# Performance work log

Measured on AMD Instinct MI355X. Metric: run time of the kernel, lower is better.

## Reference

```python
import jax, jax.numpy as jnp
import numpy as np

B, T, D = 4, 1024, 1024
H, DH = 16, 64
SCALE = 1.0 / (DH ** 0.5)


def skew(QE):
    # QE: [B, H, T, 2T-1] -> relative-position skew (Music Transformer)
    b, h, t, _ = QE.shape
    QE = jnp.pad(QE, ((0, 0), (0, 0), (0, 0), (0, 1))).reshape(b, h, 2 * t * t)
    QE = jnp.pad(QE, ((0, 0), (0, 0), (0, t - 1))).reshape(b, h, t + 1, 2 * t - 1)
    return QE[:, :, :t, -t:]


def setup_inputs() -> dict:
    key = jax.random.key(0)
    ks = jax.random.split(key, 11)
    s = 0.02
    return {
        "x": jax.random.normal(ks[0], (B, T, D), jnp.float32),
        "context": jax.random.normal(ks[1], (B, T, D), jnp.float32),
        "mask": jax.random.randint(ks[2], (B, 1, T, T), 0, 2).astype(jnp.bool_),
        "lookup_table": jax.random.normal(ks[3], (2 * T - 1, DH), jnp.float32) * s,
        "Wq": jax.random.normal(ks[4], (D, H * DH), jnp.float32) * s,
        "Wk": jax.random.normal(ks[5], (D, H * DH), jnp.float32) * s,
        "Wv": jax.random.normal(ks[6], (D, H * DH), jnp.float32) * s,
        "Wo": jax.random.normal(ks[7], (H * DH, D), jnp.float32) * s,
        "bo": jnp.zeros((D,), jnp.float32),
        "gamma": jnp.ones((D,), jnp.float32),
        "beta": jnp.zeros((D,), jnp.float32),
    }


def reference(x, context, mask, lookup_table, Wq, Wk, Wv, Wo, bo, gamma, beta):
    b, t, d = x.shape
    # projections -> [B, H, T, DH]
    q = (x @ Wq).reshape(b, t, H, DH).transpose(0, 2, 1, 3)
    k = (context @ Wk).reshape(b, t, H, DH).transpose(0, 2, 1, 3)
    v = (context @ Wv).reshape(b, t, H, DH).transpose(0, 2, 1, 3)

    score = jnp.einsum("bhqd,bhkd->bhqk", q, k)
    score = score + skew(jnp.einsum("bhqd,rd->bhqr", q, lookup_table))
    score = score * SCALE
    score = jnp.where(mask, jnp.float32(-1e9), score)
    attn = jax.nn.softmax(score, axis=-1)

    out = jnp.einsum("bhqk,bhkd->bhqd", attn, v)
    out = out.transpose(0, 2, 1, 3).reshape(b, t, H * DH)
    out = out @ Wo + bo  # dropout is identity at inference (p effectively 0)

    y = x + out
    mu = jnp.mean(y, axis=-1, keepdims=True)
    var = jnp.var(y, axis=-1, keepdims=True)
    return (y - mu) / jnp.sqrt(var + 1e-5) * gamma + beta
```

## Files before the change

kernel.cpp:

```cpp
#include <hip/hip_runtime.h>

#define Tn 1024
#define Hn 16
#define Dn 1024
#define DHn 64
#define QSCALE 0.18033688011112042f

typedef unsigned short u16;
typedef unsigned long long ull;
typedef __bf16 bf16x8 __attribute__((ext_vector_type(8)));
typedef float f32x4 __attribute__((ext_vector_type(4)));

__device__ __forceinline__ u16 f2bf(float f) {
  union { float f; unsigned u; } v; v.f = f;
  return (u16)((v.u + 0x7FFFu + ((v.u >> 16) & 1u)) >> 16);
}
__device__ __forceinline__ float bf2f(u16 s) {
  union { unsigned u; float f; } v; v.u = ((unsigned)s) << 16;
  return v.f;
}
__device__ __forceinline__ f32x4 mfma16(bf16x8 a, bf16x8 b, f32x4 c) {
  return __builtin_amdgcn_mfma_f32_16x16x32_bf16(a, b, c, 0, 0, 0);
}

__global__ void k_convert(const float* __restrict__ src, u16* __restrict__ dst, int n) {
  int i = (blockIdx.x * blockDim.x + threadIdx.x) * 4;
  if (i >= n) return;
  float4 v = *(const float4*)(src + i);
  union { u16 s[4]; uint2 u; } o;
  o.s[0] = f2bf(v.x); o.s[1] = f2bf(v.y); o.s[2] = f2bf(v.z); o.s[3] = f2bf(v.w);
  *(uint2*)(dst + i) = o.u;
}

__global__ __launch_bounds__(256) void k_maskpack(const unsigned char* __restrict__ m,
                                                  unsigned long long* __restrict__ mb) {
  int wi = blockIdx.x * 4 + (threadIdx.x >> 6);
  int lane = threadIdx.x & 63;
  unsigned char v = m[((size_t)wi << 6) + lane];
  unsigned long long bal = __ballot(v != 0);
  if (lane == 0) mb[wi] = bal;
}

__global__ void k_transpose_convert(const float* __restrict__ W, u16* __restrict__ Wt) {
  __shared__ float tile[32][33];
  int n0 = blockIdx.x * 32, k0 = blockIdx.y * 32;
  int tx = threadIdx.x, ty = threadIdx.y;
  #pragma unroll
  for (int i = 0; i < 4; i++)
    tile[ty + 8*i][tx] = W[(size_t)(k0 + ty + 8*i) * Dn + n0 + tx];
  __syncthreads();
  #pragma unroll
  for (int i = 0; i < 4; i++)
    Wt[(size_t)(n0 + ty + 8*i) * Dn + k0 + tx] = f2bf(tile[tx][ty + 8*i]);
}

__global__ __launch_bounds__(256) void k_proj(const float* __restrict__ x, const float* __restrict__ ctxI,
                                              const u16* __restrict__ WqT, const u16* __restrict__ WkvT,
                                              u16* __restrict__ Qb, u16* __restrict__ Kb, u16* __restrict__ Vb) {
  __shared__ __align__(16) u16 Al[128][40];
  __shared__ __align__(16) u16 Bl[128][40];
  int bx = blockIdx.x;
  bool isQ = bx < 256;
  int idx = isQ ? bx : bx - 256;
  int m0 = (idx & 31) * 128;
  int n0 = (idx >> 5) * 128;
  const float* A = isQ ? x : ctxI;
  const u16* Bt = isQ ? WqT : WkvT;
  u16* dst0 = isQ ? Qb : Kb;
  float scale = isQ ? QSCALE : 1.0f;
  int tid = threadIdx.x;
  int w = tid >> 6, lane = tid & 63, g = lane >> 4, lr = lane & 15;
  int wr = w >> 1, wc = w & 1;
  f32x4 acc[4][4] = {};
  int sr = tid >> 2, sc = tid & 3;
  const float* Ap0 = &A[(size_t)(m0 + sr) * Dn + sc * 8];
  const float* Ap1 = Ap0 + (size_t)64 * Dn;
  const u16* Bp0 = &Bt[(size_t)(n0 + sr) * Dn + sc * 8];
  const u16* Bp1 = Bp0 + (size_t)64 * Dn;
  float4 ra0a = *(const float4*)Ap0, ra0b = *(const float4*)(Ap0 + 4);
  float4 ra1a = *(const float4*)Ap1, ra1b = *(const float4*)(Ap1 + 4);
  int4 rb0 = *(const int4*)Bp0;
  int4 rb1 = *(const int4*)Bp1;
  for (int k0 = 0; k0 < Dn; k0 += 32) {
    __syncthreads();
    {
      union { u16 s[8]; int4 v; } c0, c1;
      c0.s[0]=f2bf(ra0a.x); c0.s[1]=f2bf(ra0a.y); c0.s[2]=f2bf(ra0a.z); c0.s[3]=f2bf(ra0a.w);
      c0.s[4]=f2bf(ra0b.x); c0.s[5]=f2bf(ra0b.y); c0.s[6]=f2bf(ra0b.z); c0.s[7]=f2bf(ra0b.w);
      c1.s[0]=f2bf(ra1a.x); c1.s[1]=f2bf(ra1a.y); c1.s[2]=f2bf(ra1a.z); c1.s[3]=f2bf(ra1a.w);
      c1.s[4]=f2bf(ra1b.x); c1.s[5]=f2bf(ra1b.y); c1.s[6]=f2bf(ra1b.z); c1.s[7]=f2bf(ra1b.w);
      *(int4*)&Al[sr][sc*8]      = c0.v;
      *(int4*)&Al[sr + 64][sc*8] = c1.v;
    }
    *(int4*)&Bl[sr][sc*8]      = rb0;
    *(int4*)&Bl[sr + 64][sc*8] = rb1;
    __syncthreads();
    if (k0 + 32 < Dn) {
      ra0a = *(const float4*)(Ap0 + k0 + 32); ra0b = *(const float4*)(Ap0 + k0 + 36);
      ra1a = *(const float4*)(Ap1 + k0 + 32); ra1b = *(const float4*)(Ap1 + k0 + 36);
      rb0 = *(const int4*)(Bp0 + k0 + 32);
      rb1 = *(const int4*)(Bp1 + k0 + 32);
    }
    bf16x8 a[4], b[4];
    #pragma unroll
    for (int mi = 0; mi < 4; mi++) a[mi] = *(const bf16x8*)&Al[wr*64 + mi*16 + lr][g*8];
    #pragma unroll
    for (int ni = 0; ni < 4; ni++) b[ni] = *(const bf16x8*)&Bl[wc*64 + ni*16 + lr][g*8];
    #pragma unroll
    for (int mi = 0; mi < 4; mi++)
      #pragma unroll
      for (int ni = 0; ni < 4; ni++)
        acc[mi][ni] = mfma16(a[mi], b[ni], acc[mi][ni]);
  }
  #pragma unroll
  for (int mi = 0; mi < 4; mi++)
    #pragma unroll
    for (int ni = 0; ni < 4; ni++) {
      int row0 = m0 + wr*64 + mi*16 + g*4;
      int col = n0 + wc*64 + ni*16 + lr;
      int bb = row0 >> 10, tt0 = row0 & 1023;
      int hh = col >> 6, dd = col & 63;
      if (hh < 16) {
        u16* p = dst0 + (((size_t)(bb*16 + hh) << 10) + (size_t)tt0) * 64 + dd;
        #pragma unroll
        for (int r = 0; r < 4; r++) p[(size_t)r * 64] = f2bf(acc[mi][ni][r] * scale);
      } else {
        union { u16 s[4]; uint2 u; } o;
        #pragma unroll
        for (int r = 0; r < 4; r++) o.s[r] = f2bf(acc[mi][ni][r]);
        *(uint2*)(Vb + (((size_t)((bb*16 + (hh - 16)) * 64 + dd)) << 10) + tt0) = o.u;
      }
    }
}

__global__ __launch_bounds__(256) void k_gemm_bt(const u16* __restrict__ A, const u16* __restrict__ Bt,
                                                 u16* __restrict__ dst0, const float* __restrict__ bias) {
  __shared__ __align__(16) u16 Al[128][40];
  __shared__ __align__(16) u16 Bl[128][40];
  int m0 = blockIdx.y * 128, n0 = blockIdx.x * 128;
  int tid = threadIdx.x;
  int w = tid >> 6, lane = tid & 63, g = lane >> 4, lr = lane & 15;
  int wr = w >> 1, wc = w & 1;
  f32x4 acc[4][4] = {};
  int sr = tid >> 2, sc = tid & 3;
  const u16* Ap0 = &A[(size_t)(m0 + sr) * Dn + sc * 8];
  const u16* Ap1 = &A[(size_t)(m0 + sr + 64) * Dn + sc * 8];
  const u16* Bp0 = &Bt[(size_t)(n0 + sr) * Dn + sc * 8];
  const u16* Bp1 = &Bt[(size_t)(n0 + sr + 64) * Dn + sc * 8];
  int4 ra0 = *(const int4*)Ap0;
  int4 ra1 = *(const int4*)Ap1;
  int4 rb0 = *(const int4*)Bp0;
  int4 rb1 = *(const int4*)Bp1;
  for (int k0 = 0; k0 < Dn; k0 += 32) {
    __syncthreads();
    *(int4*)&Al[sr][sc*8]      = ra0;
    *(int4*)&Al[sr + 64][sc*8] = ra1;
    *(int4*)&Bl[sr][sc*8]      = rb0;
    *(int4*)&Bl[sr + 64][sc*8] = rb1;
    __syncthreads();
    if (k0 + 32 < Dn) {
      ra0 = *(const int4*)(Ap0 + k0 + 32);
      ra1 = *(const int4*)(Ap1 + k0 + 32);
      rb0 = *(const int4*)(Bp0 + k0 + 32);
      rb1 = *(const int4*)(Bp1 + k0 + 32);
    }
    bf16x8 a[4], b[4];
    #pragma unroll
    for (int mi = 0; mi < 4; mi++) a[mi] = *(const bf16x8*)&Al[wr*64 + mi*16 + lr][g*8];
    #pragma unroll
    for (int ni = 0; ni < 4; ni++) b[ni] = *(const bf16x8*)&Bl[wc*64 + ni*16 + lr][g*8];
    #pragma unroll
    for (int mi = 0; mi < 4; mi++)
      #pragma unroll
      for (int ni = 0; ni < 4; ni++)
        acc[mi][ni] = mfma16(a[mi], b[ni], acc[mi][ni]);
  }
  #pragma unroll
  for (int mi = 0; mi < 4; mi++)
    #pragma unroll
    for (int ni = 0; ni < 4; ni++) {
      int row0 = m0 + wr*64 + mi*16 + g*4;
      int col = n0 + wc*64 + ni*16 + lr;
      #pragma unroll
      for (int r = 0; r < 4; r++)
        dst0[(size_t)(row0 + r) * Dn + col] = f2bf(acc[mi][ni][r] + bias[col]);
    }
}

__global__ __launch_bounds__(512, 2) void k_attn(const u16* __restrict__ Qb, const u16* __restrict__ Kb,
                                              const u16* __restrict__ VT, const u16* __restrict__ Eb,
                                              const unsigned long long* __restrict__ mbits,
                                              u16* __restrict__ ctx) {
  __shared__ __align__(16) u16 KlF[128 * 64];
  __shared__ __align__(16) u16 Vt[64][136];
  __shared__ __align__(16) u16 RP[8][16][72];
  int h = blockIdx.y;
  int b = blockIdx.x;
  int q0 = blockIdx.z * 256;
  int tid = threadIdx.x;
  int w = tid >> 6, lane = tid & 63, g = lane >> 4, lr = lane & 15;
  int qw0 = q0 + w * 32;
  size_t headoff = (size_t)(b * Hn + h) * Tn * DHn;
  bf16x8 qf0 = *(const bf16x8*)&Qb[headoff + (size_t)(qw0 + lr)*64 + g*8];
  bf16x8 qf1 = *(const bf16x8*)&Qb[headoff + (size_t)(qw0 + lr)*64 + 32 + g*8];
  bf16x8 qf2 = *(const bf16x8*)&Qb[headoff + (size_t)(qw0 + 16 + lr)*64 + g*8];
  bf16x8 qf3 = *(const bf16x8*)&Qb[headoff + (size_t)(qw0 + 16 + lr)*64 + 32 + g*8];
  f32x4 O[8] = {};
  f32x4 Os0 = {0.f, 0.f, 0.f, 0.f}, Os1 = {0.f, 0.f, 0.f, 0.f};
  union { u16 s[8]; bf16x8 v; } one8;
  #pragma unroll
  for (int j = 0; j < 8; j++) one8.s[j] = 0x3F80u;

  int srcl[4]; bool psel[4];
  #pragma unroll
  for (int r = 0; r < 4; r++) {
    int rowq = g*4 + r;
    srcl[r] = (lane & 48) + ((lr - rowq + 15) & 15);
    psel[r] = (lr <= rowq);
  }
  const unsigned long long* mrow = mbits + ((size_t)(b * Tn + qw0 + g*4) << 4);

  f32x4 carry0 = {0.f, 0.f, 0.f, 0.f}, carry1 = {0.f, 0.f, 0.f, 0.f};
  {
    int rm = 1008 - qw0;
    const u16* ep = &Eb[(size_t)(rm + lr) * 64 + g*8];
    carry0 = mfma16(qf0, *(const bf16x8*)ep, carry0);
    carry0 = mfma16(qf1, *(const bf16x8*)(ep + 32), carry0);
    const u16* ep1 = &Eb[(size_t)(rm - 16 + lr) * 64 + g*8];
    carry1 = mfma16(qf2, *(const bf16x8*)ep1, carry1);
    carry1 = mfma16(qf3, *(const bf16x8*)(ep1 + 32), carry1);
  }

  int sKr = tid >> 3, sKc = (tid & 7) * 8;
  int kswz = sKc ^ ((sKr & 7) << 3);
  int sVr = tid >> 4, sVc = (tid & 15) * 8;
  const u16* Kgs = Kb + headoff + (size_t)sKr * 64 + sKc;
  const u16* Vgs = VT + headoff + (size_t)sVr * 1024 + sVc;
  int4 kA = *(const int4*)Kgs;
  int4 kB = *(const int4*)(Kgs + (size_t)64 * 64);
  int4 vA = *(const int4*)Vgs;
  int4 vB = *(const int4*)(Vgs + 32 * 1024);

  int kread = (g * 8) ^ ((lr & 7) << 3);
  int kread2 = (32 + g * 8) ^ ((lr & 7) << 3);

  for (int k0 = 0; k0 < Tn; k0 += 128) {
    __syncthreads();
    *(int4*)&KlF[sKr * 64 + kswz]        = kA;
    *(int4*)&KlF[(sKr + 64) * 64 + kswz] = kB;
    *(int4*)&Vt[sVr][sVc]                = vA;
    *(int4*)&Vt[sVr + 32][sVc]           = vB;
    __syncthreads();

    uint2 mw0[2][4], mw1[2][4];
    #pragma unroll
    for (int t = 0; t < 2; t++)
      #pragma unroll
      for (int r = 0; r < 4; r++) {
        mw0[t][r] = *(const uint2*)(mrow + (size_t)r * 16 + (k0 >> 6) + t);
        mw1[t][r] = *(const uint2*)(mrow + 256 + (size_t)r * 16 + (k0 >> 6) + t);
      }

    int rmin0 = k0 - qw0 + 1008;
    bf16x8 pa000, pa001, pa010, pa011;
    bf16x8 pa100, pa101, pa110, pa111;

    bf16x8 e0[5][2];
    #pragma unroll
    for (int j = 0; j < 5; j++) {
      const u16* ep = &Eb[(size_t)(rmin0 + j*16 + lr) * 64 + g*8];
      e0[j][0] = *(const bf16x8*)ep;
      e0[j][1] = *(const bf16x8*)(ep + 32);
    }
    f32x4 Rm0[5], Rn0[5];
    Rm0[0] = carry0;
    Rn0[0] = carry1;
    __builtin_amdgcn_s_setprio(1);
    #pragma unroll
    for (int j = 1; j < 5; j++) {
      f32x4 R = {0.f, 0.f, 0.f, 0.f};
      R = mfma16(qf0, e0[j][0], R);
      R = mfma16(qf1, e0[j][1], R);
      Rm0[j] = R;
      f32x4 R2 = {0.f, 0.f, 0.f, 0.f};
      R2 = mfma16(qf2, e0[j-1][0], R2);
      R2 = mfma16(qf3, e0[j-1][1], R2);
      Rn0[j] = R2;
    }
    f32x4 S0[4], T0[4];
    #pragma unroll
    for (int c = 0; c < 4; c++) {
      int krow = c*16 + lr;
      bf16x8 kf0 = *(const bf16x8*)&KlF[krow*64 + kread];
      bf16x8 kf1 = *(const bf16x8*)&KlF[krow*64 + kread2];
      f32x4 z = {0.f, 0.f, 0.f, 0.f};
      z = mfma16(qf0, kf0, z); z = mfma16(qf1, kf1, z);
      S0[c] = z;
      f32x4 z2 = {0.f, 0.f, 0.f, 0.f};
      z2 = mfma16(qf2, kf0, z2); z2 = mfma16(qf3, kf1, z2);
      T0[c] = z2;
    }
    __builtin_amdgcn_s_setprio(0);
    {
      float sh[5][4], si[5][4];
      #pragma unroll
      for (int s5 = 0; s5 < 5; s5++)
        #pragma unroll
        for (int r = 0; r < 4; r++) {
          sh[s5][r] = __shfl(Rm0[s5][r], srcl[r], 64);
          si[s5][r] = __shfl(Rn0[s5][r], srcl[r], 64);
        }
      #pragma unroll
      for (int c = 0; c < 4; c++)
        #pragma unroll
        for (int r = 0; r < 4; r++) {
          float s = S0[c][r] + (psel[r] ? sh[c][r] : sh[c+1][r]);
          unsigned bit;
          if (c == 0)      bit = (mw0[0][r].x >> lr) & 1u;
          else if (c == 1) bit = (mw0[0][r].x >> (16 + lr)) & 1u;
          else if (c == 2) bit = (mw0[0][r].y >> lr) & 1u;
          else             bit = (mw0[0][r].y >> (16 + lr)) & 1u;
          s = bit ? -1e9f : s;
          RP[w][g*4 + r][c*16 + lr] = f2bf(__builtin_amdgcn_exp2f(s));
        }
      pa000 = *(const bf16x8*)&RP[w][lr][g*8];
      pa001 = *(const bf16x8*)&RP[w][lr][32 + g*8];
      #pragma unroll
      for (int c = 0; c < 4; c++)
        #pragma unroll
        for (int r = 0; r < 4; r++) {
          float s = T0[c][r] + (psel[r] ? si[c][r] : si[c+1][r]);
          unsigned bit;
          if (c == 0)      bit = (mw1[0][r].x >> lr) & 1u;
          else if (c == 1) bit = (mw1[0][r].x >> (16 + lr)) & 1u;
          else if (c == 2) bit = (mw1[0][r].y >> lr) & 1u;
          else             bit = (mw1[0][r].y >> (16 + lr)) & 1u;
          s = bit ? -1e9f : s;
          RP[w][g*4 + r][c*16 + lr] = f2bf(__builtin_amdgcn_exp2f(s));
        }
      pa010 = *(const bf16x8*)&RP[w][lr][g*8];
      pa011 = *(const bf16x8*)&RP[w][lr][32 + g*8];
    }

    bf16x8 e1[5][2];
    #pragma unroll
    for (int j = 0; j < 5; j++) {
      const u16* ep = &Eb[(size_t)(rmin0 + 64 + j*16 + lr) * 64 + g*8];
      e1[j][0] = *(const bf16x8*)ep;
      e1[j][1] = *(const bf16x8*)(ep + 32);
    }
    f32x4 Rm1[5], Rn1[5];
    Rm1[0] = Rm0[4];
    Rn1[0] = Rn0[4];
    __builtin_amdgcn_s_setprio(1);
    #pragma unroll
    for (int j = 1; j < 5; j++) {
      f32x4 R = {0.f, 0.f, 0.f, 0.f};
      R = mfma16(qf0, e1[j][0], R);
      R = mfma16(qf1, e1[j][1], R);
      Rm1[j] = R;
      f32x4 R2 = {0.f, 0.f, 0.f, 0.f};
      R2 = mfma16(qf2, e1[j-1][0], R2);
      R2 = mfma16(qf3, e1[j-1][1], R2);
      Rn1[j] = R2;
    }
    __builtin_amdgcn_s_setprio(0);
    carry0 = Rm1[4];
    carry1 = Rn1[4];

    __builtin_amdgcn_sched_barrier(0);
    if (k0 + 128 < Tn) {
      kA = *(const int4*)(Kgs + (size_t)(k0 + 128) * 64);
      kB = *(const int4*)(Kgs + (size_t)(k0 + 192) * 64);
      vA = *(const int4*)(Vgs + k0 + 128);
      vB = *(const int4*)(Vgs + 32 * 1024 + k0 + 128);
    }
    __builtin_amdgcn_sched_barrier(0);

    f32x4 S1[4], T1[4];
    __builtin_amdgcn_s_setprio(1);
    #pragma unroll
    for (int c = 0; c < 4; c++) {
      int krow = 64 + c*16 + lr;
      bf16x8 kf0 = *(const bf16x8*)&KlF[krow*64 + kread];
      bf16x8 kf1 = *(const bf16x8*)&KlF[krow*64 + kread2];
      f32x4 z = {0.f, 0.f, 0.f, 0.f};
      z = mfma16(qf0, kf0, z); z = mfma16(qf1, kf1, z);
      S1[c] = z;
      f32x4 z2 = {0.f, 0.f, 0.f, 0.f};
      z2 = mfma16(qf2, kf0, z2); z2 = mfma16(qf3, kf1, z2);
      T1[c] = z2;
    }
    __builtin_amdgcn_s_setprio(0);
    {
      float sh[5][4], si[5][4];
      #pragma unroll
      for (int s5 = 0; s5 < 5; s5++)
        #pragma unroll
        for (int r = 0; r < 4; r++) {
          sh[s5][r] = __shfl(Rm1[s5][r], srcl[r], 64);
          si[s5][r] = __shfl(Rn1[s5][r], srcl[r], 64);
        }
      #pragma unroll
      for (int c = 0; c < 4; c++)
        #pragma unroll
        for (int r = 0; r < 4; r++) {
          float s = S1[c][r] + (psel[r] ? sh[c][r] : sh[c+1][r]);
          unsigned bit;
          if (c == 0)      bit = (mw0[1][r].x >> lr) & 1u;
          else if (c == 1) bit = (mw0[1][r].x >> (16 + lr)) & 1u;
          else if (c == 2) bit = (mw0[1][r].y >> lr) & 1u;
          else             bit = (mw0[1][r].y >> (16 + lr)) & 1u;
          s = bit ? -1e9f : s;
          RP[w][g*4 + r][c*16 + lr] = f2bf(__builtin_amdgcn_exp2f(s));
        }
      pa100 = *(const bf16x8*)&RP[w][lr][g*8];
      pa101 = *(const bf16x8*)&RP[w][lr][32 + g*8];
      #pragma unroll
      for (int c = 0; c < 4; c++)
        #pragma unroll
        for (int r = 0; r < 4; r++) {
          float s = T1[c][r] + (psel[r] ? si[c][r] : si[c+1][r]);
          unsigned bit;
          if (c == 0)      bit = (mw1[1][r].x >> lr) & 1u;
          else if (c == 1) bit = (mw1[1][r].x >> (16 + lr)) & 1u;
          else if (c == 2) bit = (mw1[1][r].y >> lr) & 1u;
          else             bit = (mw1[1][r].y >> (16 + lr)) & 1u;
          s = bit ? -1e9f : s;
          RP[w][g*4 + r][c*16 + lr] = f2bf(__builtin_amdgcn_exp2f(s));
        }
      pa110 = *(const bf16x8*)&RP[w][lr][g*8];
      pa111 = *(const bf16x8*)&RP[w][lr][32 + g*8];
    }

    __builtin_amdgcn_s_setprio(1);
    #pragma unroll
    for (int ct = 0; ct < 4; ct++) {
      bf16x8 vf0 = *(const bf16x8*)&Vt[ct*16 + lr][g*8];
      bf16x8 vf1 = *(const bf16x8*)&Vt[ct*16 + lr][32 + g*8];
      bf16x8 vf2 = *(const bf16x8*)&Vt[ct*16 + lr][64 + g*8];
      bf16x8 vf3 = *(const bf16x8*)&Vt[ct*16 + lr][96 + g*8];
      O[ct] = mfma16(pa000, vf0, O[ct]);
      O[ct] = mfma16(pa001, vf1, O[ct]);
      O[ct] = mfma16(pa100, vf2, O[ct]);
      O[ct] = mfma16(pa101, vf3, O[ct]);
      O[4+ct] = mfma16(pa010, vf0, O[4+ct]);
      O[4+ct] = mfma16(pa011, vf1, O[4+ct]);
      O[4+ct] = mfma16(pa110, vf2, O[4+ct]);
      O[4+ct] = mfma16(pa111, vf3, O[4+ct]);
    }
    Os0 = mfma16(pa000, one8.v, Os0);
    Os0 = mfma16(pa001, one8.v, Os0);
    Os0 = mfma16(pa100, one8.v, Os0);
    Os0 = mfma16(pa101, one8.v, Os0);
    Os1 = mfma16(pa010, one8.v, Os1);
    Os1 = mfma16(pa011, one8.v, Os1);
    Os1 = mfma16(pa110, one8.v, Os1);
    Os1 = mfma16(pa111, one8.v, Os1);
    __builtin_amdgcn_s_setprio(0);
  }
  float inv0[4], inv1[4];
  #pragma unroll
  for (int r = 0; r < 4; r++) { inv0[r] = 1.f / Os0[r]; inv1[r] = 1.f / Os1[r]; }
  #pragma unroll
  for (int ct = 0; ct < 4; ct++)
    #pragma unroll
    for (int r = 0; r < 4; r++) {
      int rowq = g*4 + r, col = ct*16 + lr;
      ctx[(size_t)(b*Tn + qw0 + rowq) * 1024 + h*64 + col] = f2bf(O[ct][r] * inv0[r]);
      ctx[(size_t)(b*Tn + qw0 + 16 + rowq) * 1024 + h*64 + col] = f2bf(O[4+ct][r] * inv1[r]);
    }
}

__global__ __launch_bounds__(256) void k_ln(const float* __restrict__ x, const u16* __restrict__ o,
                                            const float* __restrict__ gamma, const float* __restrict__ beta,
                                            float* __restrict__ out) {
  int m = blockIdx.x, tid = threadIdx.x;
  int w = tid >> 6, lane = tid & 63;
  const float* xr = x + (size_t)m * Dn;
  const u16* orow = o + (size_t)m * Dn;
  float4 xv = *(const float4*)&xr[tid*4];
  union { uint2 u; u16 s[4]; } ou;
  ou.u = *(const uint2*)&orow[tid*4];
  float y[4];
  y[0] = xv.x + bf2f(ou.s[0]);
  y[1] = xv.y + bf2f(ou.s[1]);
  y[2] = xv.z + bf2f(ou.s[2]);
  y[3] = xv.w + bf2f(ou.s[3]);
  float s = y[0]+y[1]+y[2]+y[3];
  float s2 = y[0]*y[0]+y[1]*y[1]+y[2]*y[2]+y[3]*y[3];
  #pragma unroll
  for (int off = 1; off < 64; off <<= 1) { s += __shfl_xor(s, off); s2 += __shfl_xor(s2, off); }
  __shared__ float red[8];
  if (lane == 0) { red[w] = s; red[4 + w] = s2; }
  __syncthreads();
  float Sa = red[0]+red[1]+red[2]+red[3];
  float Sb = red[4]+red[5]+red[6]+red[7];
  float mu = Sa * (1.f/1024.f);
  float var = Sb * (1.f/1024.f) - mu*mu;
  float rstd = rsqrtf(var + 1e-5f);
  #pragma unroll
  for (int i = 0; i < 4; i++) {
    int j = tid*4 + i;
    out[(size_t)m*Dn + j] = (y[i] - mu) * rstd * gamma[j] + beta[j];
  }
}

extern "C" void kernel_launch(void* const* d_in, const int* in_sizes, int n_in,
                              void* d_out, int out_size, void* d_ws, size_t ws_size,
                              hipStream_t stream) {
  const float* x    = (const float*)d_in[0];
  const float* ctxI = (const float*)d_in[1];
  const unsigned char* mask = (const unsigned char*)d_in[2];
  const float* lut  = (const float*)d_in[3];
  const float* Wq   = (const float*)d_in[4];
  const float* Wk   = (const float*)d_in[5];
  const float* Wv   = (const float*)d_in[6];
  const float* Wo   = (const float*)d_in[7];
  const float* bo   = (const float*)d_in[8];
  const float* gamma= (const float*)d_in[9];
  const float* beta = (const float*)d_in[10];
  float* out = (float*)d_out;

  u16* WqT  = (u16*)d_ws;
  u16* WkT  = WqT + 1048576;
  u16* WvT  = WkT + 1048576;
  u16* WoT  = WvT + 1048576;
  u16* Ebf  = WoT + 1048576;
  u16* Qbf  = Ebf + 131072;
  u16* Kbf  = Qbf + 4194304;
  u16* Vbf  = Kbf + 4194304;
  u16* ctxb = Vbf + 4194304;
  u16* obf  = ctxb + 4194304;
  unsigned long long* mbits = (unsigned long long*)(obf + 4194304);

  k_maskpack<<<16384, 256, 0, stream>>>(mask, mbits);
  k_convert<<<128, 256, 0, stream>>>(lut, Ebf, 131008);
  dim3 tb(32, 8), tg(32, 32);
  k_transpose_convert<<<tg, tb, 0, stream>>>(Wq, WqT);
  k_transpose_convert<<<tg, tb, 0, stream>>>(Wk, WkT);
  k_transpose_convert<<<tg, tb, 0, stream>>>(Wv, WvT);
  k_transpose_convert<<<tg, tb, 0, stream>>>(Wo, WoT);
  k_proj<<<768, 256, 0, stream>>>(x, ctxI, WqT, WkT, Qbf, Kbf, Vbf);
  k_attn<<<dim3(4, 16, 4), 512, 0, stream>>>(Qbf, Kbf, Vbf, Ebf, mbits, ctxb);
  k_gemm_bt<<<dim3(8, 32), 256, 0, stream>>>(ctxb, WoT, obf, bo);
  k_ln<<<4096, 256, 0, stream>>>(x, obf, gamma, beta, out);
}
```

Before: 164.7 us.

## Double-buffer GEMM tiles with direct global-to-LDS loads and merge transpose launches

```diff
diff --git a/kernel.cpp b/kernel.cpp
--- a/kernel.cpp
+++ b/kernel.cpp
@@ -21,6 +21,11 @@
 }
 __device__ __forceinline__ f32x4 mfma16(bf16x8 a, bf16x8 b, f32x4 c) {
   return __builtin_amdgcn_mfma_f32_16x16x32_bf16(a, b, c, 0, 0, 0);
+}
+__device__ __forceinline__ void gload16(const u16* g, u16* l) {
+  __builtin_amdgcn_global_load_lds(
+      (const __attribute__((address_space(1))) void*)g,
+      (__attribute__((address_space(3))) void*)l, 16, 0, 0);
 }
 
 __global__ void k_convert(const float* __restrict__ src, u16* __restrict__ dst, int n) {
@@ -41,8 +46,14 @@
   if (lane == 0) mb[wi] = bal;
 }
 
-__global__ void k_transpose_convert(const float* __restrict__ W, u16* __restrict__ Wt) {
+__global__ void k_transpose_convert4(const float* __restrict__ W0, const float* __restrict__ W1,
+                                     const float* __restrict__ W2, const float* __restrict__ W3,
+                                     u16* __restrict__ T0, u16* __restrict__ T1,
+                                     u16* __restrict__ T2, u16* __restrict__ T3) {
   __shared__ float tile[32][33];
+  int z = blockIdx.z;
+  const float* W = (z == 0) ? W0 : (z == 1) ? W1 : (z == 2) ? W2 : W3;
+  u16* Wt = (z == 0) ? T0 : (z == 1) ? T1 : (z == 2) ? T2 : T3;
   int n0 = blockIdx.x * 32, k0 = blockIdx.y * 32;
   int tx = threadIdx.x, ty = threadIdx.y;
   #pragma unroll
@@ -57,8 +68,8 @@
 __global__ __launch_bounds__(256) void k_proj(const float* __restrict__ x, const float* __restrict__ ctxI,
                                               const u16* __restrict__ WqT, const u16* __restrict__ WkvT,
                                               u16* __restrict__ Qb, u16* __restrict__ Kb, u16* __restrict__ Vb) {
-  __shared__ __align__(16) u16 Al[128][40];
-  __shared__ __align__(16) u16 Bl[128][40];
+  __shared__ __align__(16) u16 AlP[2][128][40];
+  __shared__ __align__(16) u16 BlL[2][128 * 32];
   int bx = blockIdx.x;
   bool isQ = bx < 256;
   int idx = isQ ? bx : bx - 256;
@@ -75,42 +86,57 @@
   int sr = tid >> 2, sc = tid & 3;
   const float* Ap0 = &A[(size_t)(m0 + sr) * Dn + sc * 8];
   const float* Ap1 = Ap0 + (size_t)64 * Dn;
-  const u16* Bp0 = &Bt[(size_t)(n0 + sr) * Dn + sc * 8];
-  const u16* Bp1 = Bp0 + (size_t)64 * Dn;
-  float4 ra0a = *(const float4*)Ap0, ra0b = *(const float4*)(Ap0 + 4);
-  float4 ra1a = *(const float4*)Ap1, ra1b = *(const float4*)(Ap1 + 4);
-  int4 rb0 = *(const int4*)Bp0;
-  int4 rb1 = *(const int4*)Bp1;
-  for (int k0 = 0; k0 < Dn; k0 += 32) {
-    __syncthreads();
-    {
+  int srow = lane >> 2, scol = (lane & 3) * 8;
+  const u16* Bg0 = &Bt[(size_t)(n0 + w * 16 + srow) * Dn + scol];
+  const u16* Bg1 = &Bt[(size_t)(n0 + (w + 4) * 16 + srow) * Dn + scol];
+
+  float4 a0a = *(const float4*)Ap0, a0b = *(const float4*)(Ap0 + 4);
+  float4 a1a = *(const float4*)Ap1, a1b = *(const float4*)(Ap1 + 4);
+  gload16(Bg0, &BlL[0][(size_t)w * 512]);
+  gload16(Bg1, &BlL[0][(size_t)(w + 4) * 512]);
+  {
+    union { u16 s[8]; int4 v; } c0, c1;
+    c0.s[0]=f2bf(a0a.x); c0.s[1]=f2bf(a0a.y); c0.s[2]=f2bf(a0a.z); c0.s[3]=f2bf(a0a.w);
+    c0.s[4]=f2bf(a0b.x); c0.s[5]=f2bf(a0b.y); c0.s[6]=f2bf(a0b.z); c0.s[7]=f2bf(a0b.w);
+    c1.s[0]=f2bf(a1a.x); c1.s[1]=f2bf(a1a.y); c1.s[2]=f2bf(a1a.z); c1.s[3]=f2bf(a1a.w);
+    c1.s[4]=f2bf(a1b.x); c1.s[5]=f2bf(a1b.y); c1.s[6]=f2bf(a1b.z); c1.s[7]=f2bf(a1b.w);
+    *(int4*)&AlP[0][sr][sc*8]      = c0.v;
+    *(int4*)&AlP[0][sr + 64][sc*8] = c1.v;
+  }
+  a0a = *(const float4*)(Ap0 + 32); a0b = *(const float4*)(Ap0 + 36);
+  a1a = *(const float4*)(Ap1 + 32); a1b = *(const float4*)(Ap1 + 36);
+  __syncthreads();
+
+  for (int t = 0; t < 32; t++) {
+    int cur = t & 1;
+    if (t + 1 < 32) {
+      int kn = (t + 1) * 32;
+      gload16(Bg0 + kn, &BlL[cur ^ 1][(size_t)w * 512]);
+      gload16(Bg1 + kn, &BlL[cur ^ 1][(size_t)(w + 4) * 512]);
       union { u16 s[8]; int4 v; } c0, c1;
-      c0.s[0]=f2bf(ra0a.x); c0.s[1]=f2bf(ra0a.y); c0.s[2]=f2bf(ra0a.z); c0.s[3]=f2bf(ra0a.w);
-      c0.s[4]=f2bf(ra0b.x); c0.s[5]=f2bf(ra0b.y); c0.s[6]=f2bf(ra0b.z); c0.s[7]=f2bf(ra0b.w);
-      c1.s[0]=f2bf(ra1a.x); c1.s[1]=f2bf(ra1a.y); c1.s[2]=f2bf(ra1a.z); c1.s[3]=f2bf(ra1a.w);
-      c1.s[4]=f2bf(ra1b.x); c1.s[5]=f2bf(ra1b.y); c1.s[6]=f2bf(ra1b.z); c1.s[7]=f2bf(ra1b.w);
-      *(int4*)&Al[sr][sc*8]      = c0.v;
-      *(int4*)&Al[sr + 64][sc*8] = c1.v;
-    }
-    *(int4*)&Bl[sr][sc*8]      = rb0;
-    *(int4*)&Bl[sr + 64][sc*8] = rb1;
-    __syncthreads();
-    if (k0 + 32 < Dn) {
-      ra0a = *(const float4*)(Ap0 + k0 + 32); ra0b = *(const float4*)(Ap0 + k0 + 36);
-      ra1a = *(const float4*)(Ap1 + k0 + 32); ra1b = *(const float4*)(Ap1 + k0 + 36);
-      rb0 = *(const int4*)(Bp0 + k0 + 32);
-      rb1 = *(const int4*)(Bp1 + k0 + 32);
+      c0.s[0]=f2bf(a0a.x); c0.s[1]=f2bf(a0a.y); c0.s[2]=f2bf(a0a.z); c0.s[3]=f2bf(a0a.w);
+      c0.s[4]=f2bf(a0b.x); c0.s[5]=f2bf(a0b.y); c0.s[6]=f2bf(a0b.z); c0.s[7]=f2bf(a0b.w);
+      c1.s[0]=f2bf(a1a.x); c1.s[1]=f2bf(a1a.y); c1.s[2]=f2bf(a1a.z); c1.s[3]=f2bf(a1a.w);
+      c1.s[4]=f2bf(a1b.x); c1.s[5]=f2bf(a1b.y); c1.s[6]=f2bf(a1b.z); c1.s[7]=f2bf(a1b.w);
+      *(int4*)&AlP[cur ^ 1][sr][sc*8]      = c0.v;
+      *(int4*)&AlP[cur ^ 1][sr + 64][sc*8] = c1.v;
+      if (t + 2 < 32) {
+        int kf = (t + 2) * 32;
+        a0a = *(const float4*)(Ap0 + kf); a0b = *(const float4*)(Ap0 + kf + 4);
+        a1a = *(const float4*)(Ap1 + kf); a1b = *(const float4*)(Ap1 + kf + 4);
+      }
     }
     bf16x8 a[4], b[4];
     #pragma unroll
-    for (int mi = 0; mi < 4; mi++) a[mi] = *(const bf16x8*)&Al[wr*64 + mi*16 + lr][g*8];
-    #pragma unroll
-    for (int ni = 0; ni < 4; ni++) b[ni] = *(const bf16x8*)&Bl[wc*64 + ni*16 + lr][g*8];
+    for (int mi = 0; mi < 4; mi++) a[mi] = *(const bf16x8*)&AlP[cur][wr*64 + mi*16 + lr][g*8];
+    #pragma unroll
+    for (int ni = 0; ni < 4; ni++) b[ni] = *(const bf16x8*)&BlL[cur][(size_t)(wc*64 + ni*16 + lr) * 32 + g*8];
     #pragma unroll
     for (int mi = 0; mi < 4; mi++)
       #pragma unroll
       for (int ni = 0; ni < 4; ni++)
         acc[mi][ni] = mfma16(a[mi], b[ni], acc[mi][ni]);
+    __syncthreads();
   }
   #pragma unroll
   for (int mi = 0; mi < 4; mi++)
@@ -135,45 +161,45 @@
 
 __global__ __launch_bounds__(256) void k_gemm_bt(const u16* __restrict__ A, const u16* __restrict__ Bt,
                                                  u16* __restrict__ dst0, const float* __restrict__ bias) {
-  __shared__ __align__(16) u16 Al[128][40];
-  __shared__ __align__(16) u16 Bl[128][40];
+  __shared__ __align__(16) u16 AlL[2][128 * 32];
+  __shared__ __align__(16) u16 BlL[2][128 * 32];
   int m0 = blockIdx.y * 128, n0 = blockIdx.x * 128;
   int tid = threadIdx.x;
   int w = tid >> 6, lane = tid & 63, g = lane >> 4, lr = lane & 15;
   int wr = w >> 1, wc = w & 1;
   f32x4 acc[4][4] = {};
-  int sr = tid >> 2, sc = tid & 3;
-  const u16* Ap0 = &A[(size_t)(m0 + sr) * Dn + sc * 8];
-  const u16* Ap1 = &A[(size_t)(m0 + sr + 64) * Dn + sc * 8];
-  const u16* Bp0 = &Bt[(size_t)(n0 + sr) * Dn + sc * 8];
-  const u16* Bp1 = &Bt[(size_t)(n0 + sr + 64) * Dn + sc * 8];
-  int4 ra0 = *(const int4*)Ap0;
-  int4 ra1 = *(const int4*)Ap1;
-  int4 rb0 = *(const int4*)Bp0;
-  int4 rb1 = *(const int4*)Bp1;
-  for (int k0 = 0; k0 < Dn; k0 += 32) {
-    __syncthreads();
-    *(int4*)&Al[sr][sc*8]      = ra0;
-    *(int4*)&Al[sr + 64][sc*8] = ra1;
-    *(int4*)&Bl[sr][sc*8]      = rb0;
-    *(int4*)&Bl[sr + 64][sc*8] = rb1;
-    __syncthreads();
-    if (k0 + 32 < Dn) {
-      ra0 = *(const int4*)(Ap0 + k0 + 32);
-      ra1 = *(const int4*)(Ap1 + k0 + 32);
-      rb0 = *(const int4*)(Bp0 + k0 + 32);
-      rb1 = *(const int4*)(Bp1 + k0 + 32);
+  int srow = lane >> 2, scol = (lane & 3) * 8;
+  const u16* Ag0 = &A[(size_t)(m0 + w * 16 + srow) * Dn + scol];
+  const u16* Ag1 = &A[(size_t)(m0 + (w + 4) * 16 + srow) * Dn + scol];
+  const u16* Bg0 = &Bt[(size_t)(n0 + w * 16 + srow) * Dn + scol];
+  const u16* Bg1 = &Bt[(size_t)(n0 + (w + 4) * 16 + srow) * Dn + scol];
+
+  gload16(Ag0, &AlL[0][(size_t)w * 512]);
+  gload16(Ag1, &AlL[0][(size_t)(w + 4) * 512]);
+  gload16(Bg0, &BlL[0][(size_t)w * 512]);
+  gload16(Bg1, &BlL[0][(size_t)(w + 4) * 512]);
+  __syncthreads();
+
+  for (int t = 0; t < 32; t++) {
+    int cur = t & 1;
+    if (t + 1 < 32) {
+      int kn = (t + 1) * 32;
+      gload16(Ag0 + kn, &AlL[cur ^ 1][(size_t)w * 512]);
+      gload16(Ag1 + kn, &AlL[cur ^ 1][(size_t)(w + 4) * 512]);
+      gload16(Bg0 + kn, &BlL[cur ^ 1][(size_t)w * 512]);
+      gload16(Bg1 + kn, &BlL[cur ^ 1][(size_t)(w + 4) * 512]);
     }
     bf16x8 a[4], b[4];
     #pragma unroll
-    for (int mi = 0; mi < 4; mi++) a[mi] = *(const bf16x8*)&Al[wr*64 + mi*16 + lr][g*8];
-    #pragma unroll
-    for (int ni = 0; ni < 4; ni++) b[ni] = *(const bf16x8*)&Bl[wc*64 + ni*16 + lr][g*8];
+    for (int mi = 0; mi < 4; mi++) a[mi] = *(const bf16x8*)&AlL[cur][(size_t)(wr*64 + mi*16 + lr) * 32 + g*8];
+    #pragma unroll
+    for (int ni = 0; ni < 4; ni++) b[ni] = *(const bf16x8*)&BlL[cur][(size_t)(wc*64 + ni*16 + lr) * 32 + g*8];
     #pragma unroll
     for (int mi = 0; mi < 4; mi++)
       #pragma unroll
       for (int ni = 0; ni < 4; ni++)
         acc[mi][ni] = mfma16(a[mi], b[ni], acc[mi][ni]);
+    __syncthreads();
   }
   #pragma unroll
   for (int mi = 0; mi < 4; mi++)
@@ -536,11 +562,8 @@
 
   k_maskpack<<<16384, 256, 0, stream>>>(mask, mbits);
   k_convert<<<128, 256, 0, stream>>>(lut, Ebf, 131008);
-  dim3 tb(32, 8), tg(32, 32);
-  k_transpose_convert<<<tg, tb, 0, stream>>>(Wq, WqT);
-  k_transpose_convert<<<tg, tb, 0, stream>>>(Wk, WkT);
-  k_transpose_convert<<<tg, tb, 0, stream>>>(Wv, WvT);
-  k_transpose_convert<<<tg, tb, 0, stream>>>(Wo, WoT);
+  dim3 tb(32, 8), tg4(32, 32, 4);
+  k_transpose_convert4<<<tg4, tb, 0, stream>>>(Wq, Wk, Wv, Wo, WqT, WkT, WvT, WoT);
   k_proj<<<768, 256, 0, stream>>>(x, ctxI, WqT, WkT, Qbf, Kbf, Vbf);
   k_attn<<<dim3(4, 16, 4), 512, 0, stream>>>(Qbf, Kbf, Vbf, Ebf, mbits, ctxb);
   k_gemm_bt<<<dim3(8, 32), 256, 0, stream>>>(ctxb, WoT, obf, bo);
```

Measured after the change: 157.8 us. 4.2% less time.
